# Optimization experiments

Measured on AMD Instinct MI355X. Metric: run time of the kernel, lower is better.

Reference implementation:

```python
import jax, jax.numpy as jnp
import numpy as np


def _conv1x1(x, w, b):
    # x: [B,C,H,W], w: [O,C], b: [O] -> [B,O,H,W]
    return jnp.einsum('bchw,oc->bohw', x, w) + b[None, :, None, None]


def setup_inputs() -> dict:
    key = jax.random.key(0)
    ks = jax.random.split(key, 5)
    B, C, H, W = 4, 256, 64, 64
    C2 = C // 2
    scale = 0.02  # keep attention logits in a sane range
    return {
        'x': jax.random.normal(ks[0], (B, C, H, W), dtype=jnp.float32),
        'w_theta': jax.random.normal(ks[1], (C2, C), dtype=jnp.float32) * scale,
        'b_theta': jnp.zeros((C2,), dtype=jnp.float32),
        'w_phi': jax.random.normal(ks[2], (C2, C), dtype=jnp.float32) * scale,
        'b_phi': jnp.zeros((C2,), dtype=jnp.float32),
        'w_g': jax.random.normal(ks[3], (C2, C), dtype=jnp.float32) * scale,
        'b_g': jnp.zeros((C2,), dtype=jnp.float32),
        'w_out': jax.random.normal(ks[4], (C, C2), dtype=jnp.float32) * scale,
        'b_out': jnp.zeros((C,), dtype=jnp.float32),
    }


def reference(x, w_theta, b_theta, w_phi, b_phi, w_g, b_g, w_out, b_out):
    B, C, H, W = x.shape
    C2 = C // 2
    N = H * W
    theta = _conv1x1(x, w_theta, b_theta).reshape(B, C2, N)  # [B,C2,N]
    phi = _conv1x1(x, w_phi, b_phi).reshape(B, C2, N)        # [B,C2,N]
    g = _conv1x1(x, w_g, b_g).reshape(B, C2, N)              # [B,C2,N]
    # non-local attention: scores[b,m,n] = theta[b,:,m] . phi[b,:,n]
    scores = jnp.einsum('bcm,bcn->bmn', theta, phi)          # [B,N,N]
    attn = jax.nn.softmax(scores, axis=-1)                   # [B,N,N]
    # output = g @ attn^T : out[b,c,m] = sum_n g[b,c,n] * attn[b,m,n]
    out = jnp.einsum('bcn,bmn->bcm', g, attn)                # [B,C2,N]
    out = out.reshape(B, C2, H, W)
    return x + _conv1x1(out, w_out, b_out)
```

## Files before the change

kernel.cpp:

```cpp
#include <hip/hip_runtime.h>
#include <hip/hip_bf16.h>

#define B_  4
#define C_  256
#define C2_ 128
#define N_  4096
#define LOG2E 1.4426950408889634f

typedef unsigned short u16;
typedef __attribute__((ext_vector_type(8))) short bf16x8;
typedef __attribute__((ext_vector_type(4))) short s16x4;
typedef __attribute__((ext_vector_type(4))) float f32x4;

static __device__ __forceinline__ u16 f2bf(float f) {
    return __builtin_bit_cast(u16, __float2bfloat16(f));
}
static __device__ __forceinline__ float bf2f(u16 u) {
    return __bfloat162float(__builtin_bit_cast(__hip_bfloat16, u));
}
static __device__ __forceinline__ bf16x8 cvt8(const float* p) {
    u16 t[8];
#pragma unroll
    for (int j = 0; j < 8; ++j) t[j] = f2bf(p[j]);
    return *(const bf16x8*)t;
}
static __device__ __forceinline__ bf16x8 lds8(const u16* p) {
    s16x4 lo = *(const s16x4*)p;
    s16x4 hi = *(const s16x4*)(p + 4);
    return __builtin_shufflevector(lo, hi, 0, 1, 2, 3, 4, 5, 6, 7);
}
static __device__ __forceinline__ void st8(u16* p, bf16x8 v) {
    *(s16x4*)p       = __builtin_shufflevector(v, v, 0, 1, 2, 3);
    *(s16x4*)(p + 4) = __builtin_shufflevector(v, v, 4, 5, 6, 7);
}

#define XW 268

__global__ __launch_bounds__(256, 2) void projx_kernel(
    const float* __restrict__ x,
    const float* __restrict__ wt, const float* __restrict__ wp,
    const float* __restrict__ wg,
    const float* __restrict__ b_theta, const float* __restrict__ b_phi,
    const float* __restrict__ b_g,
    u16* __restrict__ Q, u16* __restrict__ K, u16* __restrict__ V) {
    __shared__ __align__(16) u16 XTs[64][XW];
    __shared__ __align__(16) u16 Ws[64][XW];
    u16 (*Vt)[72] = (u16(*)[72])XTs;

    int bid = blockIdx.x;
    int h   = bid >> 8;
    int r2  = bid & 255;
    int b   = r2 >> 6;
    int n0  = (r2 & 63) * 64;
    int tid = threadIdx.x;
    int wave = tid >> 6, lane = tid & 63, quad = (lane >> 4) & 3, l16 = lane & 15;

#pragma unroll
    for (int it = 0; it < 8; ++it) {
        int idx = it * 256 + tid;
        int q = idx & 15, p = idx >> 4;
        const float* r0 = x + ((size_t)b * C_ + 2 * p) * N_ + n0 + 4 * q;
        float4 v0 = *(const float4*)r0;
        float4 v1 = *(const float4*)(r0 + N_);
        const float* f0 = (const float*)&v0;
        const float* f1 = (const float*)&v1;
#pragma unroll
        for (int j = 0; j < 4; ++j) {
            unsigned pk = (unsigned)f2bf(f0[j]) | ((unsigned)f2bf(f1[j]) << 16);
            *(unsigned*)&XTs[4 * q + j][2 * p] = pk;
        }
    }
    __syncthreads();

    bf16x8 af[8];
#pragma unroll
    for (int ks = 0; ks < 8; ++ks)
        af[ks] = lds8(&XTs[wave * 16 + l16][ks * 32 + quad * 8]);
    __syncthreads();

    const float* wms[3]    = { wt, wp, wg };
    const float* biases[3] = { b_theta, b_phi, b_g };

#pragma unroll
    for (int mat = 0; mat < 3; ++mat) {
        const float* wm = wms[mat];
        const float* bias = biases[mat];
#pragma unroll
        for (int it = 0; it < 8; ++it) {
            int idx = it * 256 + tid;
            int row = idx >> 5, c8 = (idx & 31) * 8;
            const float* src = wm + (size_t)(h * 64 + row) * C_ + c8;
            float w8[8];
            *(float4*)&w8[0] = *(const float4*)src;
            *(float4*)&w8[4] = *(const float4*)(src + 4);
            st8(&Ws[row][c8], cvt8(w8));
        }
        __syncthreads();

        f32x4 acc[4];
#pragma unroll
        for (int i = 0; i < 4; ++i) acc[i] = (f32x4){0.f, 0.f, 0.f, 0.f};
#pragma unroll
        for (int ct = 0; ct < 4; ++ct)
#pragma unroll
            for (int ks = 0; ks < 8; ++ks) {
                bf16x8 bf = lds8(&Ws[ct * 16 + l16][ks * 32 + quad * 8]);
                acc[ct] = __builtin_amdgcn_mfma_f32_16x16x32_bf16(
                    af[ks], bf, acc[ct], 0, 0, 0);
            }

        if (mat < 2) {
            u16* dst = mat == 0 ? Q : K;
            float scl = mat == 0 ? LOG2E : 1.0f;
#pragma unroll
            for (int ct = 0; ct < 4; ++ct) {
                int c2 = h * 64 + ct * 16 + l16;
                float bb = bias[c2];
#pragma unroll
                for (int r = 0; r < 4; ++r) {
                    int n = n0 + wave * 16 + quad * 4 + r;
                    dst[((size_t)b * N_ + n) * C2_ + c2] =
                        f2bf((acc[ct][r] + bb) * scl);
                }
            }
        } else {
#pragma unroll
            for (int ct = 0; ct < 4; ++ct) {
                int c2 = h * 64 + ct * 16 + l16;
                float bb = bias[c2];
#pragma unroll
                for (int r = 0; r < 4; ++r)
                    Vt[ct * 16 + l16][wave * 16 + quad * 4 + r] =
                        f2bf(acc[ct][r] + bb);
            }
        }
        __syncthreads();
    }

#pragma unroll
    for (int it = 0; it < 2; ++it) {
        int idx = it * 256 + tid;
        int row = idx >> 3, n8 = (idx & 7) * 8;
        *(uint4*)(V + ((size_t)b * C2_ + h * 64 + row) * N_ + n0 + n8) =
            *(const uint4*)&Vt[row][n8];
    }
}

#define KS_LD 140
#define VS_LD 76
#define PS_LD 68

__global__ __launch_bounds__(256, 2) void attn_kernel(
    const u16* __restrict__ Q, const u16* __restrict__ K,
    const u16* __restrict__ V, u16* __restrict__ AO,
    u16* __restrict__ Opb, float* __restrict__ lsum, int nsplit) {
    const int BM = 128, BN = 64, D = C2_;
    const int per = B_ * (N_ / BM);
    int s    = blockIdx.x / per;
    int r0   = blockIdx.x % per;
    int b    = r0 / (N_ / BM);
    int m0   = (r0 % (N_ / BM)) * BM;
    int tid  = threadIdx.x;
    int wave = tid >> 6, lane = tid & 63, quad = (lane >> 4) & 3, l16 = lane & 15;

    __shared__ __align__(16) u16 Ks[BN][KS_LD];
    __shared__ __align__(16) u16 Vs[C2_][VS_LD];
    u16* Ps = &Ks[0][0] + wave * (32 * PS_LD);

    bf16x8 qf[2][4];
#pragma unroll
    for (int ms = 0; ms < 2; ++ms) {
        const u16* qp = Q + ((size_t)b * N_ + m0 + wave * 32 + ms * 16 + l16) * D;
#pragma unroll
        for (int kk = 0; kk < 4; ++kk)
            qf[ms][kk] = *(const bf16x8*)(qp + kk * 32 + quad * 8);
    }

    float l_r[2][4] = {{0.f, 0.f, 0.f, 0.f}, {0.f, 0.f, 0.f, 0.f}};
    f32x4 o_acc[2][8];
#pragma unroll
    for (int ms = 0; ms < 2; ++ms)
#pragma unroll
        for (int i = 0; i < 8; ++i) o_acc[ms][i] = (f32x4){0.f, 0.f, 0.f, 0.f};

    const int tiles = N_ / BN;
    const int base = tiles / nsplit, rem = tiles % nsplit;
    const int t0 = s * base + (s < rem ? s : rem);
    const int cnt = base + (s < rem ? 1 : 0);
    const int nt0 = t0 * BN, nt1 = (t0 + cnt) * BN;

    for (int nt = nt0; nt < nt1; nt += BN) {
        const u16* kp = K + ((size_t)b * N_ + nt) * D;
#pragma unroll
        for (int it = 0; it < 4; ++it) {
            int idx = it * 256 + tid;
            int row = idx >> 4, col = (idx & 15) * 8;
            uint4 raw = *(const uint4*)(kp + row * D + col);
            *(uint2*)&Ks[row][col]     = make_uint2(raw.x, raw.y);
            *(uint2*)&Ks[row][col + 4] = make_uint2(raw.z, raw.w);
        }
#pragma unroll
        for (int it = 0; it < 4; ++it) {
            int idx = it * 256 + tid;
            int row = idx >> 3, col = (idx & 7) * 8;
            uint4 raw = *(const uint4*)(V + ((size_t)b * C2_ + row) * N_ + nt + col);
            *(uint2*)&Vs[row][col]     = make_uint2(raw.x, raw.y);
            *(uint2*)&Vs[row][col + 4] = make_uint2(raw.z, raw.w);
        }
        __syncthreads();

        unsigned pkd[2][4][2];
#pragma unroll
        for (int nn = 0; nn < 4; ++nn) {
            f32x4 a0 = (f32x4){0.f, 0.f, 0.f, 0.f};
            f32x4 a1 = (f32x4){0.f, 0.f, 0.f, 0.f};
#pragma unroll
            for (int kk = 0; kk < 4; ++kk) {
                bf16x8 kf = lds8(&Ks[nn * 16 + l16][kk * 32 + quad * 8]);
                a0 = __builtin_amdgcn_mfma_f32_16x16x32_bf16(qf[0][kk], kf, a0, 0, 0, 0);
                a1 = __builtin_amdgcn_mfma_f32_16x16x32_bf16(qf[1][kk], kf, a1, 0, 0, 0);
            }
#pragma unroll
            for (int rp = 0; rp < 2; ++rp) {
                float p0 = __builtin_amdgcn_exp2f(a0[2 * rp]);
                float p1 = __builtin_amdgcn_exp2f(a0[2 * rp + 1]);
                l_r[0][2 * rp]     += p0;
                l_r[0][2 * rp + 1] += p1;
                pkd[0][nn][rp] = (unsigned)f2bf(p0) | ((unsigned)f2bf(p1) << 16);
                float p2 = __builtin_amdgcn_exp2f(a1[2 * rp]);
                float p3 = __builtin_amdgcn_exp2f(a1[2 * rp + 1]);
                l_r[1][2 * rp]     += p2;
                l_r[1][2 * rp + 1] += p3;
                pkd[1][nn][rp] = (unsigned)f2bf(p2) | ((unsigned)f2bf(p3) << 16);
            }
        }

        __syncthreads();

#pragma unroll
        for (int ms = 0; ms < 2; ++ms)
#pragma unroll
            for (int nn = 0; nn < 4; ++nn)
#pragma unroll
                for (int rp = 0; rp < 2; ++rp) {
                    unsigned v = pkd[ms][nn][rp];
                    int rb = (ms * 16 + quad * 4 + 2 * rp) * PS_LD + nn * 16 + l16;
                    Ps[rb]         = (u16)v;
                    Ps[rb + PS_LD] = (u16)(v >> 16);
                }

#pragma unroll
        for (int ks = 0; ks < 2; ++ks) {
            bf16x8 pf0 = lds8(Ps + l16 * PS_LD + ks * 32 + quad * 8);
            bf16x8 pf1 = lds8(Ps + (16 + l16) * PS_LD + ks * 32 + quad * 8);
#pragma unroll
            for (int cs = 0; cs < 8; ++cs) {
                bf16x8 vf = lds8(&Vs[cs * 16 + l16][ks * 32 + quad * 8]);
                o_acc[0][cs] = __builtin_amdgcn_mfma_f32_16x16x32_bf16(pf0, vf, o_acc[0][cs], 0, 0, 0);
                o_acc[1][cs] = __builtin_amdgcn_mfma_f32_16x16x32_bf16(pf1, vf, o_acc[1][cs], 0, 0, 0);
            }
        }
        __syncthreads();
    }

#pragma unroll
    for (int ms = 0; ms < 2; ++ms)
#pragma unroll
        for (int r = 0; r < 4; ++r) {
            l_r[ms][r] += __shfl_xor(l_r[ms][r], 1);
            l_r[ms][r] += __shfl_xor(l_r[ms][r], 2);
            l_r[ms][r] += __shfl_xor(l_r[ms][r], 4);
            l_r[ms][r] += __shfl_xor(l_r[ms][r], 8);
        }

    if (Opb) {
#pragma unroll
        for (int ms = 0; ms < 2; ++ms) {
#pragma unroll
            for (int cs = 0; cs < 8; ++cs)
#pragma unroll
                for (int r = 0; r < 4; ++r) {
                    size_t row = (size_t)s * (B_ * N_) + (size_t)b * N_ +
                                 m0 + wave * 32 + ms * 16 + quad * 4 + r;
                    Opb[row * C2_ + cs * 16 + l16] = f2bf(o_acc[ms][cs][r]);
                }
            if (l16 == 0)
#pragma unroll
                for (int r = 0; r < 4; ++r) {
                    size_t row = (size_t)s * (B_ * N_) + (size_t)b * N_ +
                                 m0 + wave * 32 + ms * 16 + quad * 4 + r;
                    lsum[row] = l_r[ms][r];
                }
        }
    } else {
#pragma unroll
        for (int ms = 0; ms < 2; ++ms)
#pragma unroll
            for (int cs = 0; cs < 8; ++cs)
#pragma unroll
                for (int r = 0; r < 4; ++r) {
                    float v = o_acc[ms][cs][r] / l_r[ms][r];
                    AO[((size_t)b * N_ + m0 + wave * 32 + ms * 16 + quad * 4 + r) * C2_ +
                       cs * 16 + l16] = f2bf(v);
                }
    }
}

#define OW 140

__global__ __launch_bounds__(256, 4) void outproj_kernel(
    const float* __restrict__ x, const u16* __restrict__ Opb,
    const float* __restrict__ lsum, const u16* __restrict__ AO,
    const float* __restrict__ w_out, const float* __restrict__ b_out,
    float* __restrict__ y, int nsplit) {
    __shared__ __align__(16) u16 As[64][OW];
    __shared__ __align__(16) u16 Ws2[64][OW];
    __shared__ float Ls[64];
    int bid = blockIdx.x;
    int per_b = (C_ / 64) * (N_ / 64);
    int b   = bid / per_b;
    int rem = bid % per_b;
    int c0  = (rem / (N_ / 64)) * 64;
    int n0  = (rem % (N_ / 64)) * 64;
    int tid = threadIdx.x;
    int wave = tid >> 6, lane = tid & 63, quad = (lane >> 4) & 3, l16 = lane & 15;

#pragma unroll
    for (int it = 0; it < 4; ++it) {
        int idx = it * 256 + tid;
        int row = idx >> 4, c8 = (idx & 15) * 8;
        const float* src = w_out + (size_t)(c0 + row) * C2_ + c8;
        float w8[8];
        *(float4*)&w8[0] = *(const float4*)src;
        *(float4*)&w8[4] = *(const float4*)(src + 4);
        st8(&Ws2[row][c8], cvt8(w8));
    }

    if (nsplit > 1) {
        if (tid < 64) {
            float L = 0.f;
            for (int s = 0; s < nsplit; ++s)
                L += lsum[(size_t)s * (B_ * N_) + (size_t)b * N_ + n0 + tid];
            Ls[tid] = 1.f / L;
        }
        __syncthreads();
#pragma unroll
        for (int it = 0; it < 4; ++it) {
            int idx = it * 256 + tid;
            int n = idx >> 4, c8 = (idx & 15) * 8;
            float a[8] = {0.f, 0.f, 0.f, 0.f, 0.f, 0.f, 0.f, 0.f};
            for (int s = 0; s < nsplit; ++s) {
                const u16* op = Opb +
                    ((size_t)s * (B_ * N_) + (size_t)b * N_ + n0 + n) * C2_ + c8;
                uint4 raw = *(const uint4*)op;
                const u16* rp = (const u16*)&raw;
#pragma unroll
                for (int j = 0; j < 8; ++j) a[j] += bf2f(rp[j]);
            }
            float inv = Ls[n];
            u16 o[8];
#pragma unroll
            for (int j = 0; j < 8; ++j) o[j] = f2bf(a[j] * inv);
            st8(&As[n][c8], *(const bf16x8*)o);
        }
    } else {
#pragma unroll
        for (int it = 0; it < 4; ++it) {
            int idx = it * 256 + tid;
            int n = idx >> 4, c8 = (idx & 15) * 8;
            uint4 raw = *(const uint4*)(AO + ((size_t)b * N_ + n0 + n) * C2_ + c8);
            *(uint2*)&As[n][c8]     = make_uint2(raw.x, raw.y);
            *(uint2*)&As[n][c8 + 4] = make_uint2(raw.z, raw.w);
        }
    }
    __syncthreads();

    bf16x8 af[4];
#pragma unroll
    for (int kk = 0; kk < 4; ++kk)
        af[kk] = lds8(&Ws2[wave * 16 + l16][kk * 32 + quad * 8]);

    f32x4 acc[4];
#pragma unroll
    for (int i = 0; i < 4; ++i) acc[i] = (f32x4){0.f, 0.f, 0.f, 0.f};

#pragma unroll
    for (int nn = 0; nn < 4; ++nn)
#pragma unroll
        for (int kk = 0; kk < 4; ++kk) {
            bf16x8 bf = lds8(&As[nn * 16 + l16][kk * 32 + quad * 8]);
            acc[nn] = __builtin_amdgcn_mfma_f32_16x16x32_bf16(af[kk], bf, acc[nn], 0, 0, 0);
        }

    int cw = c0 + wave * 16;
    float bo[4];
#pragma unroll
    for (int r = 0; r < 4; ++r) bo[r] = b_out[cw + quad * 4 + r];

#pragma unroll
    for (int nn = 0; nn < 4; ++nn)
#pragma unroll
        for (int r = 0; r < 4; ++r) {
            int c = cw + quad * 4 + r;
            size_t off = ((size_t)b * C_ + c) * N_ + n0 + nn * 16 + l16;
            y[off] = x[off] + bo[r] + acc[nn][r];
        }
}

extern "C" void kernel_launch(void* const* d_in, const int* in_sizes, int n_in,
                              void* d_out, int out_size, void* d_ws, size_t ws_size,
                              hipStream_t stream) {
    const float* x       = (const float*)d_in[0];
    const float* w_theta = (const float*)d_in[1];
    const float* b_theta = (const float*)d_in[2];
    const float* w_phi   = (const float*)d_in[3];
    const float* b_phi   = (const float*)d_in[4];
    const float* w_g     = (const float*)d_in[5];
    const float* b_g     = (const float*)d_in[6];
    const float* w_out   = (const float*)d_in[7];
    const float* b_out   = (const float*)d_in[8];
    float* y = (float*)d_out;

    const size_t SZ = (size_t)B_ * N_ * C2_;
    u16* Q = (u16*)d_ws;
    u16* K = Q + SZ;
    u16* V = K + SZ;
    char* dyn = (char*)(V + SZ);
    size_t fixedB = 3 * SZ * 2;

    size_t perS = SZ * 2 + (size_t)B_ * N_ * 4;

    int S;
    if      (ws_size >= fixedB + 8 * perS) S = 8;
    else if (ws_size >= fixedB + 4 * perS) S = 4;
    else if (ws_size >= fixedB + 2 * perS) S = 2;
    else                                   S = 1;

    u16*   AO  = (u16*)dyn;
    u16*   Opb = nullptr;
    float* ls  = nullptr;
    if (S > 1) {
        Opb = (u16*)dyn;
        ls  = (float*)(Opb + (size_t)S * SZ);
    }

    projx_kernel<<<B_ * (N_ / 64) * 2, 256, 0, stream>>>(
        x, w_theta, w_phi, w_g, b_theta, b_phi, b_g, Q, K, V);
    attn_kernel<<<B_ * (N_ / 128) * S, 256, 0, stream>>>(Q, K, V, AO, Opb, ls, S);
    outproj_kernel<<<B_ * (C_ / 64) * (N_ / 64), 256, 0, stream>>>(
        x, Opb, ls, AO, w_out, b_out, y, S);
}
```

Measured before the change: 160.3 us.

## Pre-convert weights to bf16 once, separate P buffer in attention, cap split at 4

Adds a small prep kernel that converts all projection and output weights to bf16 once per call. The projection and out-projection kernels then read those bf16 fragments straight from global memory instead of staging fp32 weights through LDS, which removes shared memory and barriers. The attention kernel gets its own per-wave P buffer, so exp results are written to LDS directly and the extra barrier that protected reuse of the K tile is gone. The key-split count is capped at 4 instead of 8. The cost is one extra kernel launch, more LDS in the attention kernel (which may lower occupancy), and fewer blocks from the smaller split.

```diff
diff --git a/kernel.cpp b/kernel.cpp
--- a/kernel.cpp
+++ b/kernel.cpp
@@ -29,22 +29,36 @@
     s16x4 hi = *(const s16x4*)(p + 4);
     return __builtin_shufflevector(lo, hi, 0, 1, 2, 3, 4, 5, 6, 7);
 }
-static __device__ __forceinline__ void st8(u16* p, bf16x8 v) {
-    *(s16x4*)p       = __builtin_shufflevector(v, v, 0, 1, 2, 3);
-    *(s16x4*)(p + 4) = __builtin_shufflevector(v, v, 4, 5, 6, 7);
+
+__global__ __launch_bounds__(256) void prep_kernel(
+    const float* __restrict__ wt, const float* __restrict__ wp,
+    const float* __restrict__ wg, const float* __restrict__ wo,
+    u16* __restrict__ Wb, u16* __restrict__ Wob) {
+    int g = (blockIdx.x * 256 + threadIdx.x) * 8;
+    const float* src;
+    u16* dst;
+    if (g < 3 * 32768) {
+        int mat = g >> 15;
+        src = (mat == 0 ? wt : mat == 1 ? wp : wg) + (g & 32767);
+        dst = Wb + g;
+    } else {
+        src = wo + (g & 32767);
+        dst = Wob + (g & 32767);
+    }
+    float w8[8];
+    *(float4*)&w8[0] = *(const float4*)src;
+    *(float4*)&w8[4] = *(const float4*)(src + 4);
+    *(bf16x8*)dst = cvt8(w8);
 }
 
 #define XW 268
 
 __global__ __launch_bounds__(256, 2) void projx_kernel(
-    const float* __restrict__ x,
-    const float* __restrict__ wt, const float* __restrict__ wp,
-    const float* __restrict__ wg,
+    const float* __restrict__ x, const u16* __restrict__ Wb,
     const float* __restrict__ b_theta, const float* __restrict__ b_phi,
     const float* __restrict__ b_g,
     u16* __restrict__ Q, u16* __restrict__ K, u16* __restrict__ V) {
     __shared__ __align__(16) u16 XTs[64][XW];
-    __shared__ __align__(16) u16 Ws[64][XW];
     u16 (*Vt)[72] = (u16(*)[72])XTs;
 
     int bid = blockIdx.x;
@@ -78,36 +92,28 @@
         af[ks] = lds8(&XTs[wave * 16 + l16][ks * 32 + quad * 8]);
     __syncthreads();
 
-    const float* wms[3]    = { wt, wp, wg };
     const float* biases[3] = { b_theta, b_phi, b_g };
 
 #pragma unroll
     for (int mat = 0; mat < 3; ++mat) {
-        const float* wm = wms[mat];
         const float* bias = biases[mat];
-#pragma unroll
-        for (int it = 0; it < 8; ++it) {
-            int idx = it * 256 + tid;
-            int row = idx >> 5, c8 = (idx & 31) * 8;
-            const float* src = wm + (size_t)(h * 64 + row) * C_ + c8;
-            float w8[8];
-            *(float4*)&w8[0] = *(const float4*)src;
-            *(float4*)&w8[4] = *(const float4*)(src + 4);
-            st8(&Ws[row][c8], cvt8(w8));
-        }
-        __syncthreads();
-
         f32x4 acc[4];
 #pragma unroll
         for (int i = 0; i < 4; ++i) acc[i] = (f32x4){0.f, 0.f, 0.f, 0.f};
-#pragma unroll
-        for (int ct = 0; ct < 4; ++ct)
-#pragma unroll
-            for (int ks = 0; ks < 8; ++ks) {
-                bf16x8 bf = lds8(&Ws[ct * 16 + l16][ks * 32 + quad * 8]);
+
+#pragma unroll
+        for (int ct = 0; ct < 4; ++ct) {
+            const u16* wrow = Wb + mat * 32768 +
+                              (size_t)(h * 64 + ct * 16 + l16) * 256 + quad * 8;
+            bf16x8 bfr[8];
+#pragma unroll
+            for (int ks = 0; ks < 8; ++ks)
+                bfr[ks] = *(const bf16x8*)(wrow + ks * 32);
+#pragma unroll
+            for (int ks = 0; ks < 8; ++ks)
                 acc[ct] = __builtin_amdgcn_mfma_f32_16x16x32_bf16(
-                    af[ks], bf, acc[ct], 0, 0, 0);
-            }
+                    af[ks], bfr[ks], acc[ct], 0, 0, 0);
+        }
 
         if (mat < 2) {
             u16* dst = mat == 0 ? Q : K;
@@ -134,8 +140,8 @@
                         f2bf(acc[ct][r] + bb);
             }
         }
-        __syncthreads();
-    }
+    }
+    __syncthreads();
 
 #pragma unroll
     for (int it = 0; it < 2; ++it) {
@@ -165,7 +171,8 @@
 
     __shared__ __align__(16) u16 Ks[BN][KS_LD];
     __shared__ __align__(16) u16 Vs[C2_][VS_LD];
-    u16* Ps = &Ks[0][0] + wave * (32 * PS_LD);
+    __shared__ __align__(16) u16 Psb[4][32][PS_LD];
+    u16* Ps = &Psb[wave][0][0];
 
     bf16x8 qf[2][4];
 #pragma unroll
@@ -209,7 +216,6 @@
         }
         __syncthreads();
 
-        unsigned pkd[2][4][2];
 #pragma unroll
         for (int nn = 0; nn < 4; ++nn) {
             f32x4 a0 = (f32x4){0.f, 0.f, 0.f, 0.f};
@@ -221,33 +227,15 @@
                 a1 = __builtin_amdgcn_mfma_f32_16x16x32_bf16(qf[1][kk], kf, a1, 0, 0, 0);
             }
 #pragma unroll
-            for (int rp = 0; rp < 2; ++rp) {
-                float p0 = __builtin_amdgcn_exp2f(a0[2 * rp]);
-                float p1 = __builtin_amdgcn_exp2f(a0[2 * rp + 1]);
-                l_r[0][2 * rp]     += p0;
-                l_r[0][2 * rp + 1] += p1;
-                pkd[0][nn][rp] = (unsigned)f2bf(p0) | ((unsigned)f2bf(p1) << 16);
-                float p2 = __builtin_amdgcn_exp2f(a1[2 * rp]);
-                float p3 = __builtin_amdgcn_exp2f(a1[2 * rp + 1]);
-                l_r[1][2 * rp]     += p2;
-                l_r[1][2 * rp + 1] += p3;
-                pkd[1][nn][rp] = (unsigned)f2bf(p2) | ((unsigned)f2bf(p3) << 16);
-            }
-        }
-
-        __syncthreads();
-
-#pragma unroll
-        for (int ms = 0; ms < 2; ++ms)
-#pragma unroll
-            for (int nn = 0; nn < 4; ++nn)
-#pragma unroll
-                for (int rp = 0; rp < 2; ++rp) {
-                    unsigned v = pkd[ms][nn][rp];
-                    int rb = (ms * 16 + quad * 4 + 2 * rp) * PS_LD + nn * 16 + l16;
-                    Ps[rb]         = (u16)v;
-                    Ps[rb + PS_LD] = (u16)(v >> 16);
-                }
+            for (int r = 0; r < 4; ++r) {
+                float p0 = __builtin_amdgcn_exp2f(a0[r]);
+                float p1 = __builtin_amdgcn_exp2f(a1[r]);
+                l_r[0][r] += p0;
+                l_r[1][r] += p1;
+                Ps[(quad * 4 + r) * PS_LD + nn * 16 + l16]        = f2bf(p0);
+                Ps[(16 + quad * 4 + r) * PS_LD + nn * 16 + l16]   = f2bf(p1);
+            }
+        }
 
 #pragma unroll
         for (int ks = 0; ks < 2; ++ks) {
@@ -311,10 +299,9 @@
 __global__ __launch_bounds__(256, 4) void outproj_kernel(
     const float* __restrict__ x, const u16* __restrict__ Opb,
     const float* __restrict__ lsum, const u16* __restrict__ AO,
-    const float* __restrict__ w_out, const float* __restrict__ b_out,
+    const u16* __restrict__ Wob, const float* __restrict__ b_out,
     float* __restrict__ y, int nsplit) {
     __shared__ __align__(16) u16 As[64][OW];
-    __shared__ __align__(16) u16 Ws2[64][OW];
     __shared__ float Ls[64];
     int bid = blockIdx.x;
     int per_b = (C_ / 64) * (N_ / 64);
@@ -325,16 +312,11 @@
     int tid = threadIdx.x;
     int wave = tid >> 6, lane = tid & 63, quad = (lane >> 4) & 3, l16 = lane & 15;
 
-#pragma unroll
-    for (int it = 0; it < 4; ++it) {
-        int idx = it * 256 + tid;
-        int row = idx >> 4, c8 = (idx & 15) * 8;
-        const float* src = w_out + (size_t)(c0 + row) * C2_ + c8;
-        float w8[8];
-        *(float4*)&w8[0] = *(const float4*)src;
-        *(float4*)&w8[4] = *(const float4*)(src + 4);
-        st8(&Ws2[row][c8], cvt8(w8));
-    }
+    bf16x8 af[4];
+#pragma unroll
+    for (int kk = 0; kk < 4; ++kk)
+        af[kk] = *(const bf16x8*)(Wob + (size_t)(c0 + wave * 16 + l16) * C2_ +
+                                  kk * 32 + quad * 8);
 
     if (nsplit > 1) {
         if (tid < 64) {
@@ -361,7 +343,8 @@
             u16 o[8];
 #pragma unroll
             for (int j = 0; j < 8; ++j) o[j] = f2bf(a[j] * inv);
-            st8(&As[n][c8], *(const bf16x8*)o);
+            *(s16x4*)&As[n][c8]     = *(const s16x4*)&o[0];
+            *(s16x4*)&As[n][c8 + 4] = *(const s16x4*)&o[4];
         }
     } else {
 #pragma unroll
@@ -374,11 +357,6 @@
         }
     }
     __syncthreads();
-
-    bf16x8 af[4];
-#pragma unroll
-    for (int kk = 0; kk < 4; ++kk)
-        af[kk] = lds8(&Ws2[wave * 16 + l16][kk * 32 + quad * 8]);
 
     f32x4 acc[4];
 #pragma unroll
@@ -422,17 +400,18 @@
     float* y = (float*)d_out;
 
     const size_t SZ = (size_t)B_ * N_ * C2_;
-    u16* Q = (u16*)d_ws;
-    u16* K = Q + SZ;
-    u16* V = K + SZ;
-    char* dyn = (char*)(V + SZ);
-    size_t fixedB = 3 * SZ * 2;
+    u16* Q   = (u16*)d_ws;
+    u16* K   = Q + SZ;
+    u16* V   = K + SZ;
+    u16* Wb  = V + SZ;
+    u16* Wob = Wb + 3 * 32768;
+    char* dyn = (char*)(Wob + 32768);
+    size_t fixedB = (3 * SZ + 4 * 32768) * 2;
 
     size_t perS = SZ * 2 + (size_t)B_ * N_ * 4;
 
     int S;
-    if      (ws_size >= fixedB + 8 * perS) S = 8;
-    else if (ws_size >= fixedB + 4 * perS) S = 4;
+    if      (ws_size >= fixedB + 4 * perS) S = 4;
     else if (ws_size >= fixedB + 2 * perS) S = 2;
     else                                   S = 1;
 
@@ -444,9 +423,10 @@
         ls  = (float*)(Opb + (size_t)S * SZ);
     }
 
+    prep_kernel<<<64, 256, 0, stream>>>(w_theta, w_phi, w_g, w_out, Wb, Wob);
     projx_kernel<<<B_ * (N_ / 64) * 2, 256, 0, stream>>>(
-        x, w_theta, w_phi, w_g, b_theta, b_phi, b_g, Q, K, V);
+        x, Wb, b_theta, b_phi, b_g, Q, K, V);
     attn_kernel<<<B_ * (N_ / 128) * S, 256, 0, stream>>>(Q, K, V, AO, Opb, ls, S);
     outproj_kernel<<<B_ * (C_ / 64) * (N_ / 64), 256, 0, stream>>>(
-        x, Opb, ls, AO, w_out, b_out, y, S);
-}
+        x, Opb, ls, AO, Wob, b_out, y, S);
+}
```

Measured after the change: 168.9 us. 5.4% more time.
